# Performance work log

Hardware: AMD Instinct MI355X
Metric: run time of the kernel (lower is better)

Reference implementation:

```python
import jax, jax.numpy as jnp
import numpy as np

D_MODEL = 1024
NUM_HEADS = 16
D_K = D_MODEL // NUM_HEADS


def setup_inputs() -> dict:
    key = jax.random.key(0)
    ks = jax.random.split(key, 11)
    B, S = 4, 2048
    s = 1.0 / np.sqrt(D_MODEL)
    inp = {
        "q": jax.random.normal(ks[0], (B, S, D_MODEL), jnp.float32),
        "k": jax.random.normal(ks[1], (B, S, D_MODEL), jnp.float32),
        "v": jax.random.normal(ks[2], (B, S, D_MODEL), jnp.float32),
        "w_q": jax.random.normal(ks[3], (D_MODEL, D_MODEL), jnp.float32) * s,
        "b_q": jnp.zeros((D_MODEL,), jnp.float32),
        "w_k": jax.random.normal(ks[4], (D_MODEL, D_MODEL), jnp.float32) * s,
        "b_k": jnp.zeros((D_MODEL,), jnp.float32),
        "w_v": jax.random.normal(ks[5], (D_MODEL, D_MODEL), jnp.float32) * s,
        "b_v": jnp.zeros((D_MODEL,), jnp.float32),
        "w_o": jax.random.normal(ks[6], (D_MODEL, D_MODEL), jnp.float32) * s,
        "b_o": jnp.zeros((D_MODEL,), jnp.float32),
    }
    return inp


def reference(q, k, v, w_q, b_q, w_k, b_k, w_v, b_v, w_o, b_o):
    B, S, _ = q.shape
    # projections; weights stored as [in, out] so x @ W + b
    def proj(x, w, b):
        y = x @ w + b  # [B, S, d_model]
        return y.reshape(B, -1, NUM_HEADS, D_K).transpose(0, 2, 1, 3)  # [B,H,S,d_k]
    qh = proj(q, w_q, b_q)
    kh = proj(k, w_k, b_k)
    vh = proj(v, w_v, b_v)
    scores = jnp.einsum("bhsd,bhtd->bhst", qh, kh) / jnp.sqrt(jnp.float32(D_K))
    attn = jax.nn.softmax(scores, axis=-1)  # dropout p=0.0 -> identity
    x = jnp.einsum("bhst,bhtd->bhsd", attn, vh)
    x = x.transpose(0, 2, 1, 3).reshape(B, S, D_MODEL)
    return x @ w_o + b_o
```

## Files before the change

### kernel.cpp

```cpp
#include <hip/hip_runtime.h>
#include <hip/hip_bf16.h>
#include <stdint.h>

#define D_MODEL 1024
#define SEQ 2048
#define BATCH 4
#define NHEADS 16
#define ROWS (BATCH*SEQ)

#define QKSCALE 0.18033688011f
#define DEFER_THR 11.5f

typedef __attribute__((ext_vector_type(4))) float f32x4;
typedef __attribute__((ext_vector_type(8))) short short8;
typedef __attribute__((ext_vector_type(4))) unsigned int uint4v;

#if __has_builtin(__builtin_amdgcn_exp2f)
#define EXP2(x) __builtin_amdgcn_exp2f(x)
#else
#define EXP2(x) exp2f(x)
#endif

__device__ __forceinline__ unsigned short f2bf(float f) {
    unsigned int x = __builtin_bit_cast(unsigned int, f);
    x += 0x7fffu + ((x >> 16) & 1u);
    return (unsigned short)(x >> 16);
}

__device__ __forceinline__ unsigned int cvtpk(float a, float b) {
    unsigned int r;
    asm("v_cvt_pk_bf16_f32 %0, %1, %2" : "=v"(r) : "v"(a), "v"(b));
    return r;
}

__global__ __launch_bounds__(256) void wtrans_kernel(const float* __restrict__ w,
                                                     unsigned short* __restrict__ wt) {
    __shared__ float tile[32][33];
    int tx = threadIdx.x & 31;
    int ty = threadIdx.x >> 5;
    int r0 = blockIdx.y * 32, c0 = blockIdx.x * 32;
    #pragma unroll
    for (int i = 0; i < 4; ++i)
        tile[ty + 8*i][tx] = w[(size_t)(r0 + ty + 8*i) * D_MODEL + (c0 + tx)];
    __syncthreads();
    int t = threadIdx.x;
    if (t < 128) {
        int n_loc = t >> 2;
        int kc = t & 3;
        int n = c0 + n_loc;
        int kbase = r0 + kc*8;
        uint4v pk;
        #pragma unroll
        for (int j = 0; j < 4; ++j)
            pk[j] = cvtpk(tile[kc*8 + 2*j][n_loc], tile[kc*8 + 2*j + 1][n_loc]);
        size_t tidx = (size_t)(n >> 7) * 16 + (kbase >> 6);
        int row = n & 127;
        int byte = (row*128 + (kbase & 63)*2) ^ ((row & 7) << 4);
        *(uint4v*)((char*)wt + tidx*16384 + byte) = pk;
    }
}

template<int AF32, int OUTMODE, int QSCALE>
__global__ __launch_bounds__(256) void gemm_kernel(const void* __restrict__ Aptr,
                                                   const unsigned short* __restrict__ Bt,
                                                   const float* __restrict__ bias,
                                                   void* __restrict__ Out) {
    __shared__ __attribute__((aligned(16))) unsigned short Alds[2][128*64];
    __shared__ __attribute__((aligned(16))) unsigned short Blds[2][128*64];
    const int m0 = blockIdx.x * 128;
    const int n0 = blockIdx.y * 128;
    const int t = threadIdx.x;
    const int lane = t & 63;
    const int w = t >> 6;
    const int wm = w >> 1, wn = w & 1;
    const int l15 = lane & 15, lg = lane >> 4;

    const float* Af = (const float*)Aptr;
    const unsigned short* Ab = (const unsigned short*)Aptr;
    const int arow = t >> 3;
    const int acb = ((t & 7) * 16) ^ ((arow & 7) << 4);

    f32x4 acc[4][4];
    #pragma unroll
    for (int i = 0; i < 4; ++i)
        #pragma unroll
        for (int j = 0; j < 4; ++j) acc[i][j] = (f32x4)(0.0f);

    if (AF32) {
        #pragma unroll
        for (int i = 0; i < 8; ++i) {
            int idx = t + i*256;
            int row = idx >> 4, c4 = idx & 15;
            f32x4 v = *(const f32x4*)(Af + (size_t)(m0+row)*D_MODEL + c4*4);
            unsigned long long pk = (unsigned long long)cvtpk(v[0], v[1])
                                  | ((unsigned long long)cvtpk(v[2], v[3]) << 32);
            int byte = (row*128 + c4*8) ^ ((row & 7) << 4);
            *(unsigned long long*)((char*)Alds[0] + byte) = pk;
        }
    } else {
        #pragma unroll
        for (int i = 0; i < 4; ++i) {
            const char* src = (const char*)(Ab + (size_t)(m0 + arow + i*32)*D_MODEL) + acb;
            __builtin_amdgcn_global_load_lds(
                (const __attribute__((address_space(1))) void*)src,
                (__attribute__((address_space(3))) void*)(Alds[0] + t*8 + i*2048),
                16, 0, 0);
        }
    }
    {
        const unsigned short* tsrc = Bt + ((size_t)(n0 >> 7) * 16 + 0) * 8192;
        #pragma unroll
        for (int i = 0; i < 4; ++i)
            __builtin_amdgcn_global_load_lds(
                (const __attribute__((address_space(1))) void*)(tsrc + t*8 + i*2048),
                (__attribute__((address_space(3))) void*)(Blds[0] + t*8 + i*2048),
                16, 0, 0);
    }
    __syncthreads();

    #pragma unroll 2
    for (int kt = 0; kt < 16; ++kt) {
        const int cur = kt & 1, nxt = cur ^ 1;
        const int k0n = (kt + 1) * 64;
        f32x4 av[8];
        if (kt < 15) {
            if (AF32) {
                #pragma unroll
                for (int i = 0; i < 8; ++i) {
                    int idx = t + i*256;
                    int row = idx >> 4, c4 = idx & 15;
                    av[i] = *(const f32x4*)(Af + (size_t)(m0+row)*D_MODEL + k0n + c4*4);
                }
            } else {
                #pragma unroll
                for (int i = 0; i < 4; ++i) {
                    const char* src = (const char*)(Ab + (size_t)(m0 + arow + i*32)*D_MODEL + k0n) + acb;
                    __builtin_amdgcn_global_load_lds(
                        (const __attribute__((address_space(1))) void*)src,
                        (__attribute__((address_space(3))) void*)(Alds[nxt] + t*8 + i*2048),
                        16, 0, 0);
                }
            }
            const unsigned short* tsrc = Bt + ((size_t)(n0 >> 7) * 16 + (k0n >> 6)) * 8192;
            #pragma unroll
            for (int i = 0; i < 4; ++i)
                __builtin_amdgcn_global_load_lds(
                    (const __attribute__((address_space(1))) void*)(tsrc + t*8 + i*2048),
                    (__attribute__((address_space(3))) void*)(Blds[nxt] + t*8 + i*2048),
                    16, 0, 0);
        }

        #pragma unroll
        for (int kk = 0; kk < 2; ++kk) {
            short8 af[4], bfr[4];
            #pragma unroll
            for (int mi = 0; mi < 4; ++mi) {
                int row = wm*64 + mi*16 + l15;
                int byte = (row*128 + kk*64 + lg*16) ^ ((row & 7) << 4);
                af[mi] = *(const short8*)((const char*)Alds[cur] + byte);
            }
            #pragma unroll
            for (int ni = 0; ni < 4; ++ni) {
                int row = wn*64 + ni*16 + l15;
                int byte = (row*128 + kk*64 + lg*16) ^ ((row & 7) << 4);
                bfr[ni] = *(const short8*)((const char*)Blds[cur] + byte);
            }
            #pragma unroll
            for (int mi = 0; mi < 4; ++mi)
                #pragma unroll
                for (int ni = 0; ni < 4; ++ni)
                    acc[mi][ni] = __builtin_amdgcn_mfma_f32_16x16x32_bf16(
                        af[mi], bfr[ni], acc[mi][ni], 0, 0, 0);
        }

        if (AF32 && kt < 15) {
            #pragma unroll
            for (int i = 0; i < 8; ++i) {
                int idx = t + i*256;
                int row = idx >> 4, c4 = idx & 15;
                unsigned long long pk = (unsigned long long)cvtpk(av[i][0], av[i][1])
                                      | ((unsigned long long)cvtpk(av[i][2], av[i][3]) << 32);
                int byte = (row*128 + c4*8) ^ ((row & 7) << 4);
                *(unsigned long long*)((char*)Alds[nxt] + byte) = pk;
            }
        }
        __syncthreads();
    }

    #pragma unroll
    for (int mi = 0; mi < 4; ++mi)
        #pragma unroll
        for (int ni = 0; ni < 4; ++ni) {
            int col = n0 + wn*64 + ni*16 + l15;
            float bv = bias[col];
            if (OUTMODE == 2) {
                int h = col >> 6, d = col & 63;
                int row0 = m0 + wm*64 + mi*16 + lg*4;
                int bb = row0 >> 11, s = row0 & 2047;
                unsigned long long pk = 0;
                #pragma unroll
                for (int r = 0; r < 4; ++r) {
                    float v = acc[mi][ni][r] + bv;
                    pk |= (unsigned long long)f2bf(v) << (16*r);
                }
                *(unsigned long long*)((unsigned short*)Out
                    + ((size_t)((bb*NHEADS + h)*64 + d))*SEQ + s) = pk;
            } else {
                #pragma unroll
                for (int r = 0; r < 4; ++r) {
                    int row = m0 + wm*64 + mi*16 + lg*4 + r;
                    float v = acc[mi][ni][r] + bv;
                    if (QSCALE) v *= QKSCALE;
                    if (OUTMODE == 1) {
                        int bb = row >> 11, s = row & 2047;
                        int h = col >> 6, d = col & 63;
                        ((unsigned short*)Out)[(((size_t)(bb*NHEADS + h)*SEQ + s) << 6) + d] = f2bf(v);
                    } else {
                        ((float*)Out)[(size_t)row*D_MODEL + col] = v;
                    }
                }
            }
        }
}

__global__ __launch_bounds__(256, 4) void attn_kernel(const unsigned short* __restrict__ qh,
                                                      const unsigned short* __restrict__ kh,
                                                      const unsigned short* __restrict__ vt,
                                                      unsigned short* __restrict__ xout) {
    __shared__ __attribute__((aligned(16))) unsigned short Klds[2][64*64];
    __shared__ __attribute__((aligned(16))) unsigned short Vtl[2][64*64];

    const int qb = blockIdx.x;
    const int bh = blockIdx.y;
    const int t = threadIdx.x;
    const int lane = t & 63;
    const int w = t >> 6;
    const int l15 = lane & 15, lg = lane >> 4;

    const unsigned short* qbase = qh + (size_t)bh * SEQ * 64;
    const unsigned short* kbase = kh + (size_t)bh * SEQ * 64;
    const unsigned short* vtbase = vt + (size_t)bh * 64 * SEQ;

    short8 qf[2][2];
    #pragma unroll
    for (int l = 0; l < 2; ++l) {
        int qrow = qb*128 + w*32 + l*16 + l15;
        qf[l][0] = *(const short8*)(qbase + (size_t)qrow*64 + lg*8);
        qf[l][1] = *(const short8*)(qbase + (size_t)qrow*64 + 32 + lg*8);
    }

    const int c8 = t & 7;
    const int r0 = t >> 3;
    const int r1 = r0 + 32;
    const int p0 = (r0 & 0x23) | ((r0 & 4) << 2) | ((r0 & 0x18) >> 1);
    const int p1 = (r1 & 0x23) | ((r1 & 4) << 2) | ((r1 & 0x18) >> 1);
    const int kb0 = (p0*128 + c8*16) ^ ((p0 & 7) << 4);
    const int kb1 = (p1*128 + c8*16) ^ ((p1 & 7) << 4);
    const int vb0 = (r0*128 + c8*16) ^ ((r0 & 7) << 4);
    const int vb1 = (r1*128 + c8*16) ^ ((r1 & 7) << 4);
    const unsigned short* kg0 = kbase + r0*64 + c8*8;
    const unsigned short* kg1 = kbase + r1*64 + c8*8;
    const unsigned short* vg0 = vtbase + (size_t)r0*SEQ + c8*8;
    const unsigned short* vg1 = vtbase + (size_t)r1*SEQ + c8*8;

    int fb[4][2];
    #pragma unroll
    for (int nb = 0; nb < 4; ++nb) {
        int rr = nb*16 + l15;
        int sw = (rr & 7) << 4;
        fb[nb][0] = (rr*128 + lg*16) ^ sw;
        fb[nb][1] = (rr*128 + 64 + lg*16) ^ sw;
    }

    float m[2] = {-1e30f, -1e30f}, lsum[2] = {0.f, 0.f};
    f32x4 o[2][4];
    #pragma unroll
    for (int l = 0; l < 2; ++l)
        #pragma unroll
        for (int nb = 0; nb < 4; ++nb) o[l][nb] = (f32x4)(0.0f);

    short8 kr0 = *(const short8*)(kg0);
    short8 kr1 = *(const short8*)(kg1);
    short8 vr0 = *(const short8*)(vg0);
    short8 vr1 = *(const short8*)(vg1);
    *(short8*)((char*)Klds[0] + kb0) = kr0;
    *(short8*)((char*)Klds[0] + kb1) = kr1;
    *(short8*)((char*)Vtl[0] + vb0) = vr0;
    *(short8*)((char*)Vtl[0] + vb1) = vr1;
    __syncthreads();

    const int NT = SEQ/64;
    #pragma unroll 2
    for (int ti = 0; ti < NT; ++ti) {
        const int c = ti & 1;
        if (ti + 1 < NT) {
            int off = (ti + 1) * 64;
            kr0 = *(const short8*)(kg0 + (size_t)off*64);
            kr1 = *(const short8*)(kg1 + (size_t)off*64);
            vr0 = *(const short8*)(vg0 + off);
            vr1 = *(const short8*)(vg1 + off);
        }
        const char* Kc = (const char*)Klds[c];
        const char* Vc = (const char*)Vtl[c];

        f32x4 s4[2][4];
        #pragma unroll
        for (int nb = 0; nb < 4; ++nb) {
            short8 kf0 = *(const short8*)(Kc + fb[nb][0]);
            short8 kf1 = *(const short8*)(Kc + fb[nb][1]);
            __builtin_amdgcn_s_setprio(1);
            #pragma unroll
            for (int l = 0; l < 2; ++l) {
                f32x4 s = (f32x4)(0.0f);
                s = __builtin_amdgcn_mfma_f32_16x16x32_bf16(kf0, qf[l][0], s, 0, 0, 0);
                s = __builtin_amdgcn_mfma_f32_16x16x32_bf16(kf1, qf[l][1], s, 0, 0, 0);
                s4[l][nb] = s;
            }
            __builtin_amdgcn_s_setprio(0);
        }

        union U { short8 s; unsigned int u[4]; } pa[2][2];
        #pragma unroll
        for (int l = 0; l < 2; ++l) {
            float p[16];
            float ts = 0.f;
            #pragma unroll
            for (int nb = 0; nb < 4; ++nb)
                #pragma unroll
                for (int r = 0; r < 4; ++r) {
                    float pv = EXP2(s4[l][nb][r] - m[l]);
                    p[nb*4 + r] = pv;
                    ts += pv;
                }

            float tm = s4[l][0][0];
            #pragma unroll
            for (int nb = 0; nb < 4; ++nb)
                #pragma unroll
                for (int r = 0; r < 4; ++r) tm = fmaxf(tm, s4[l][nb][r]);
            tm = fmaxf(tm, __shfl_xor(tm, 16));
            tm = fmaxf(tm, __shfl_xor(tm, 32));

            if (__any(tm > m[l] + DEFER_THR)) {
                float mnew = fmaxf(m[l], tm);
                float alpha = EXP2(m[l] - mnew);
                lsum[l] *= alpha;
                m[l] = mnew;
                #pragma unroll
                for (int r = 0; r < 4; ++r) {
                    float ar = __shfl(alpha, lg*4 + r);
                    #pragma unroll
                    for (int nb = 0; nb < 4; ++nb) o[l][nb][r] *= ar;
                }
                ts = 0.f;
                #pragma unroll
                for (int nb = 0; nb < 4; ++nb)
                    #pragma unroll
                    for (int r = 0; r < 4; ++r) {
                        float pv = EXP2(s4[l][nb][r] - m[l]);
                        p[nb*4 + r] = pv;
                        ts += pv;
                    }
            }
            lsum[l] += ts;

            pa[l][0].u[0] = cvtpk(p[0],  p[1]);  pa[l][0].u[1] = cvtpk(p[2],  p[3]);
            pa[l][0].u[2] = cvtpk(p[4],  p[5]);  pa[l][0].u[3] = cvtpk(p[6],  p[7]);
            pa[l][1].u[0] = cvtpk(p[8],  p[9]);  pa[l][1].u[1] = cvtpk(p[10], p[11]);
            pa[l][1].u[2] = cvtpk(p[12], p[13]); pa[l][1].u[3] = cvtpk(p[14], p[15]);
        }

        #pragma unroll
        for (int nb = 0; nb < 4; ++nb) {
            short8 vf0 = *(const short8*)(Vc + fb[nb][0]);
            short8 vf1 = *(const short8*)(Vc + fb[nb][1]);
            __builtin_amdgcn_s_setprio(1);
            o[0][nb] = __builtin_amdgcn_mfma_f32_16x16x32_bf16(pa[0][0].s, vf0, o[0][nb], 0, 0, 0);
            o[0][nb] = __builtin_amdgcn_mfma_f32_16x16x32_bf16(pa[0][1].s, vf1, o[0][nb], 0, 0, 0);
            o[1][nb] = __builtin_amdgcn_mfma_f32_16x16x32_bf16(pa[1][0].s, vf0, o[1][nb], 0, 0, 0);
            o[1][nb] = __builtin_amdgcn_mfma_f32_16x16x32_bf16(pa[1][1].s, vf1, o[1][nb], 0, 0, 0);
            __builtin_amdgcn_s_setprio(0);
        }

        if (ti + 1 < NT) {
            *(short8*)((char*)Klds[c^1] + kb0) = kr0;
            *(short8*)((char*)Klds[c^1] + kb1) = kr1;
            *(short8*)((char*)Vtl[c^1] + vb0) = vr0;
            *(short8*)((char*)Vtl[c^1] + vb1) = vr1;
        }
        __syncthreads();
    }

    const int bb = bh >> 4, h = bh & 15;
    #pragma unroll
    for (int l = 0; l < 2; ++l) {
        float lt = lsum[l];
        lt += __shfl_xor(lt, 16);
        lt += __shfl_xor(lt, 32);
        float rl[4];
        #pragma unroll
        for (int r = 0; r < 4; ++r) rl[r] = 1.0f / __shfl(lt, lg*4 + r);
        #pragma unroll
        for (int nb = 0; nb < 4; ++nb)
            #pragma unroll
            for (int r = 0; r < 4; ++r) {
                int s = qb*128 + w*32 + l*16 + lg*4 + r;
                int d = nb*16 + l15;
                xout[((size_t)(bb*SEQ + s))*D_MODEL + h*64 + d] = f2bf(o[l][nb][r] * rl[r]);
            }
    }
}

extern "C" void kernel_launch(void* const* d_in, const int* in_sizes, int n_in,
                              void* d_out, int out_size, void* d_ws, size_t ws_size,
                              hipStream_t stream) {
    (void)in_sizes; (void)n_in; (void)out_size; (void)ws_size;
    const float* q  = (const float*)d_in[0];
    const float* k  = (const float*)d_in[1];
    const float* v  = (const float*)d_in[2];
    const float* wq = (const float*)d_in[3];
    const float* bq = (const float*)d_in[4];
    const float* wk = (const float*)d_in[5];
    const float* bk = (const float*)d_in[6];
    const float* wv = (const float*)d_in[7];
    const float* bv = (const float*)d_in[8];
    const float* wo = (const float*)d_in[9];
    const float* bo = (const float*)d_in[10];

    char* ws = (char*)d_ws;
    unsigned short* wqt = (unsigned short*)(ws);
    unsigned short* wkt = (unsigned short*)(ws + (2ull << 20));
    unsigned short* wvt = (unsigned short*)(ws + (4ull << 20));
    unsigned short* wot = (unsigned short*)(ws + (6ull << 20));
    unsigned short* qhd = (unsigned short*)(ws + (8ull << 20));
    unsigned short* khd = (unsigned short*)(ws + (24ull << 20));
    unsigned short* vtd = (unsigned short*)(ws + (40ull << 20));
    unsigned short* xat = (unsigned short*)(ws + (56ull << 20));

    dim3 tgrid(D_MODEL/32, D_MODEL/32);
    hipLaunchKernelGGL(wtrans_kernel, tgrid, dim3(256), 0, stream, wq, wqt);
    hipLaunchKernelGGL(wtrans_kernel, tgrid, dim3(256), 0, stream, wk, wkt);
    hipLaunchKernelGGL(wtrans_kernel, tgrid, dim3(256), 0, stream, wv, wvt);
    hipLaunchKernelGGL(wtrans_kernel, tgrid, dim3(256), 0, stream, wo, wot);

    dim3 ggrid(ROWS/128, D_MODEL/128);
    hipLaunchKernelGGL((gemm_kernel<1,1,1>), ggrid, dim3(256), 0, stream,
                       (const void*)q, wqt, bq, (void*)qhd);
    hipLaunchKernelGGL((gemm_kernel<1,1,0>), ggrid, dim3(256), 0, stream,
                       (const void*)k, wkt, bk, (void*)khd);
    hipLaunchKernelGGL((gemm_kernel<1,2,0>), ggrid, dim3(256), 0, stream,
                       (const void*)v, wvt, bv, (void*)vtd);

    hipLaunchKernelGGL(attn_kernel, dim3(SEQ/128, BATCH*NHEADS), dim3(256), 0, stream,
                       qhd, khd, vtd, xat);

    hipLaunchKernelGGL((gemm_kernel<0,0,0>), ggrid, dim3(256), 0, stream,
                       (const void*)xat, wot, bo, d_out);
}
```

Measured before the change: 213.7 us.

## Pre-swizzle K/V into LDS tile images and stream them with global_load_lds

The K and V projection epilogues now write their outputs directly in the swizzled, per-64-row tile layout that the attention kernel keeps in LDS. The attention kernel can then copy each tile with global_load_lds, bypassing registers and dropping the separate register-to-LDS store step. The attention grid is also remapped so blocks for the same batch-head land on the same XCD, which should improve L2 reuse. The softmax now skips the per-tile max reduction and rescales only when the running sum overflows. That removes reductions and shuffles from each tile, but the probabilities can grow very large, which risks precision.

```diff
diff --git a/kernel.cpp b/kernel.cpp
--- a/kernel.cpp
+++ b/kernel.cpp
@@ -9,7 +9,6 @@
 #define ROWS (BATCH*SEQ)
 
 #define QKSCALE 0.18033688011f
-#define DEFER_THR 11.5f
 
 typedef __attribute__((ext_vector_type(4))) float f32x4;
 typedef __attribute__((ext_vector_type(8))) short short8;
@@ -196,15 +195,28 @@
             if (OUTMODE == 2) {
                 int h = col >> 6, d = col & 63;
                 int row0 = m0 + wm*64 + mi*16 + lg*4;
-                int bb = row0 >> 11, s = row0 & 2047;
+                int bb = row0 >> 11, s0 = row0 & 2047;
+                int ti = s0 >> 6, kvl0 = s0 & 63;
                 unsigned long long pk = 0;
                 #pragma unroll
+                for (int r = 0; r < 4; ++r)
+                    pk |= (unsigned long long)f2bf(acc[mi][ni][r] + bv) << (16*r);
+                int byte = (d*128 + kvl0*2) ^ ((d & 7) << 4);
+                *(unsigned long long*)((char*)Out
+                    + ((size_t)(bb*NHEADS + h)*32 + ti)*8192 + byte) = pk;
+            } else if (OUTMODE == 3) {
+                int h = col >> 6, d = col & 63;
+                #pragma unroll
                 for (int r = 0; r < 4; ++r) {
-                    float v = acc[mi][ni][r] + bv;
-                    pk |= (unsigned long long)f2bf(v) << (16*r);
-                }
-                *(unsigned long long*)((unsigned short*)Out
-                    + ((size_t)((bb*NHEADS + h)*64 + d))*SEQ + s) = pk;
+                    int row = m0 + wm*64 + mi*16 + lg*4 + r;
+                    int bb = row >> 11, s = row & 2047;
+                    int ti = s >> 6, kvl = s & 63;
+                    int ph = (kvl & 0x23) | ((kvl & 4) << 2) | ((kvl & 0x18) >> 1);
+                    int byte = (ph*128 + d*2) ^ ((ph & 7) << 4);
+                    *(unsigned short*)((char*)Out
+                        + ((size_t)(bb*NHEADS + h)*32 + ti)*8192 + byte)
+                        = f2bf(acc[mi][ni][r] + bv);
+                }
             } else {
                 #pragma unroll
                 for (int r = 0; r < 4; ++r) {
@@ -224,22 +236,24 @@
 }
 
 __global__ __launch_bounds__(256, 4) void attn_kernel(const unsigned short* __restrict__ qh,
-                                                      const unsigned short* __restrict__ kh,
-                                                      const unsigned short* __restrict__ vt,
+                                                      const unsigned short* __restrict__ kimg_all,
+                                                      const unsigned short* __restrict__ vimg_all,
                                                       unsigned short* __restrict__ xout) {
     __shared__ __attribute__((aligned(16))) unsigned short Klds[2][64*64];
     __shared__ __attribute__((aligned(16))) unsigned short Vtl[2][64*64];
 
-    const int qb = blockIdx.x;
-    const int bh = blockIdx.y;
+    const int bid = blockIdx.x;
+    const int xcd = bid & 7, idx = bid >> 3;
+    const int qb = idx >> 3;
+    const int bh = ((idx & 7) << 3) | xcd;
     const int t = threadIdx.x;
     const int lane = t & 63;
     const int w = t >> 6;
     const int l15 = lane & 15, lg = lane >> 4;
 
     const unsigned short* qbase = qh + (size_t)bh * SEQ * 64;
-    const unsigned short* kbase = kh + (size_t)bh * SEQ * 64;
-    const unsigned short* vtbase = vt + (size_t)bh * 64 * SEQ;
+    const unsigned short* kimg = kimg_all + (size_t)bh * SEQ * 64;
+    const unsigned short* vimg = vimg_all + (size_t)bh * SEQ * 64;
 
     short8 qf[2][2];
     #pragma unroll
@@ -248,20 +262,6 @@
         qf[l][0] = *(const short8*)(qbase + (size_t)qrow*64 + lg*8);
         qf[l][1] = *(const short8*)(qbase + (size_t)qrow*64 + 32 + lg*8);
     }
-
-    const int c8 = t & 7;
-    const int r0 = t >> 3;
-    const int r1 = r0 + 32;
-    const int p0 = (r0 & 0x23) | ((r0 & 4) << 2) | ((r0 & 0x18) >> 1);
-    const int p1 = (r1 & 0x23) | ((r1 & 4) << 2) | ((r1 & 0x18) >> 1);
-    const int kb0 = (p0*128 + c8*16) ^ ((p0 & 7) << 4);
-    const int kb1 = (p1*128 + c8*16) ^ ((p1 & 7) << 4);
-    const int vb0 = (r0*128 + c8*16) ^ ((r0 & 7) << 4);
-    const int vb1 = (r1*128 + c8*16) ^ ((r1 & 7) << 4);
-    const unsigned short* kg0 = kbase + r0*64 + c8*8;
-    const unsigned short* kg1 = kbase + r1*64 + c8*8;
-    const unsigned short* vg0 = vtbase + (size_t)r0*SEQ + c8*8;
-    const unsigned short* vg1 = vtbase + (size_t)r1*SEQ + c8*8;
 
     int fb[4][2];
     #pragma unroll
@@ -279,14 +279,15 @@
         #pragma unroll
         for (int nb = 0; nb < 4; ++nb) o[l][nb] = (f32x4)(0.0f);
 
-    short8 kr0 = *(const short8*)(kg0);
-    short8 kr1 = *(const short8*)(kg1);
-    short8 vr0 = *(const short8*)(vg0);
-    short8 vr1 = *(const short8*)(vg1);
-    *(short8*)((char*)Klds[0] + kb0) = kr0;
-    *(short8*)((char*)Klds[0] + kb1) = kr1;
-    *(short8*)((char*)Vtl[0] + vb0) = vr0;
-    *(short8*)((char*)Vtl[0] + vb1) = vr1;
+    #pragma unroll
+    for (int i = 0; i < 2; ++i) {
+        __builtin_amdgcn_global_load_lds(
+            (const __attribute__((address_space(1))) void*)(kimg + t*8 + i*2048),
+            (__attribute__((address_space(3))) void*)(Klds[0] + t*8 + i*2048), 16, 0, 0);
+        __builtin_amdgcn_global_load_lds(
+            (const __attribute__((address_space(1))) void*)(vimg + t*8 + i*2048),
+            (__attribute__((address_space(3))) void*)(Vtl[0] + t*8 + i*2048), 16, 0, 0);
+    }
     __syncthreads();
 
     const int NT = SEQ/64;
@@ -294,11 +295,17 @@
     for (int ti = 0; ti < NT; ++ti) {
         const int c = ti & 1;
         if (ti + 1 < NT) {
-            int off = (ti + 1) * 64;
-            kr0 = *(const short8*)(kg0 + (size_t)off*64);
-            kr1 = *(const short8*)(kg1 + (size_t)off*64);
-            vr0 = *(const short8*)(vg0 + off);
-            vr1 = *(const short8*)(vg1 + off);
+            const unsigned short* ks = kimg + (size_t)(ti + 1)*4096;
+            const unsigned short* vs = vimg + (size_t)(ti + 1)*4096;
+            #pragma unroll
+            for (int i = 0; i < 2; ++i) {
+                __builtin_amdgcn_global_load_lds(
+                    (const __attribute__((address_space(1))) void*)(ks + t*8 + i*2048),
+                    (__attribute__((address_space(3))) void*)(Klds[c^1] + t*8 + i*2048), 16, 0, 0);
+                __builtin_amdgcn_global_load_lds(
+                    (const __attribute__((address_space(1))) void*)(vs + t*8 + i*2048),
+                    (__attribute__((address_space(3))) void*)(Vtl[c^1] + t*8 + i*2048), 16, 0, 0);
+            }
         }
         const char* Kc = (const char*)Klds[c];
         const char* Vc = (const char*)Vtl[c];
@@ -333,15 +340,14 @@
                     ts += pv;
                 }
 
-            float tm = s4[l][0][0];
-            #pragma unroll
-            for (int nb = 0; nb < 4; ++nb)
-                #pragma unroll
-                for (int r = 0; r < 4; ++r) tm = fmaxf(tm, s4[l][nb][r]);
-            tm = fmaxf(tm, __shfl_xor(tm, 16));
-            tm = fmaxf(tm, __shfl_xor(tm, 32));
-
-            if (__any(tm > m[l] + DEFER_THR)) {
+            if (__any(!(ts < 1e30f))) {
+                float tm = s4[l][0][0];
+                #pragma unroll
+                for (int nb = 0; nb < 4; ++nb)
+                    #pragma unroll
+                    for (int r = 0; r < 4; ++r) tm = fmaxf(tm, s4[l][nb][r]);
+                tm = fmaxf(tm, __shfl_xor(tm, 16));
+                tm = fmaxf(tm, __shfl_xor(tm, 32));
                 float mnew = fmaxf(m[l], tm);
                 float alpha = EXP2(m[l] - mnew);
                 lsum[l] *= alpha;
@@ -382,12 +388,6 @@
             __builtin_amdgcn_s_setprio(0);
         }
 
-        if (ti + 1 < NT) {
-            *(short8*)((char*)Klds[c^1] + kb0) = kr0;
-            *(short8*)((char*)Klds[c^1] + kb1) = kr1;
-            *(short8*)((char*)Vtl[c^1] + vb0) = vr0;
-            *(short8*)((char*)Vtl[c^1] + vb1) = vr1;
-        }
         __syncthreads();
     }
 
@@ -446,12 +446,12 @@
     dim3 ggrid(ROWS/128, D_MODEL/128);
     hipLaunchKernelGGL((gemm_kernel<1,1,1>), ggrid, dim3(256), 0, stream,
                        (const void*)q, wqt, bq, (void*)qhd);
-    hipLaunchKernelGGL((gemm_kernel<1,1,0>), ggrid, dim3(256), 0, stream,
+    hipLaunchKernelGGL((gemm_kernel<1,3,0>), ggrid, dim3(256), 0, stream,
                        (const void*)k, wkt, bk, (void*)khd);
     hipLaunchKernelGGL((gemm_kernel<1,2,0>), ggrid, dim3(256), 0, stream,
                        (const void*)v, wvt, bv, (void*)vtd);
 
-    hipLaunchKernelGGL(attn_kernel, dim3(SEQ/128, BATCH*NHEADS), dim3(256), 0, stream,
+    hipLaunchKernelGGL(attn_kernel, dim3(16*64), dim3(256), 0, stream,
                        qhd, khd, vtd, xat);
 
     hipLaunchKernelGGL((gemm_kernel<0,0,0>), ggrid, dim3(256), 0, stream,
```

After: 199.4 us. 1.07x faster.
